# Optimization experiments

Measured on AMD Instinct MI355X. Metric: run time of the kernel, lower is better.

The kernel has to match this reference:

```python
import jax, jax.numpy as jnp
import numpy as np

N, C, H, W = 4, 256, 32, 32
NH = 2                      # att_nhead
HD = C // NH                # 128 per-head dim
MAX_DIS = 7
WS = 2 * MAX_DIS + 1        # 15 window side
WW = WS * WS                # 225 window positions
T = (C / NH) ** 0.5


def _gather_idx(h, w):
    # idx[wpos, m]: flat index into zero-padded (h+14, w+14) grid of the
    # neighbor at window offset wpos for query pixel m (== F.unfold semantics)
    pw = w + 2 * MAX_DIS
    dy, dx = np.meshgrid(np.arange(WS), np.arange(WS), indexing='ij')
    ys, xs = np.meshgrid(np.arange(h), np.arange(w), indexing='ij')
    idx = (dy.reshape(-1, 1) + ys.reshape(1, -1)) * pw + (dx.reshape(-1, 1) + xs.reshape(1, -1))
    return jnp.asarray(idx, dtype=jnp.int32)  # [WW, h*w]


def setup_inputs() -> dict:
    key = jax.random.key(0)
    ks = jax.random.split(key, 14)
    s = 0.02
    return {
        'q': jax.random.normal(ks[0], (N, C, H, W), jnp.float32),
        'k': jax.random.normal(ks[1], (N, C, H, W), jnp.float32),
        'v': jax.random.normal(ks[2], (N, C, H, W), jnp.float32),
        'Wq': jax.random.normal(ks[3], (C, C), jnp.float32) * s,
        'bq': jnp.zeros((C,), jnp.float32),
        'Wk': jax.random.normal(ks[4], (C, C), jnp.float32) * s,
        'bk': jnp.zeros((C,), jnp.float32),
        'Wv': jax.random.normal(ks[5], (C, C), jnp.float32) * s,
        'bv': jnp.zeros((C,), jnp.float32),
        'Wrel': jax.random.normal(ks[6], (NH, WW, HD), jnp.float32) * s,   # grouped 1x1 conv
        'brel': jnp.zeros((NH * WW,), jnp.float32),
        'V_bias': jax.random.normal(ks[7], (NH, HD, WW), jnp.float32) * s,
        'Wfc': jax.random.normal(ks[8], (C, C), jnp.float32) * s,
        'bfc': jnp.zeros((C,), jnp.float32),
    }


def _conv1x1(x, Wt, b):
    return jnp.einsum('nchw,dc->ndhw', x, Wt) + b[None, :, None, None]


def reference(q, k, v, Wq, bq, Wk, bk, Wv, bv, Wrel, brel, V_bias, Wfc, bfc):
    n, c, h, w = q.shape
    hw = h * w
    idx = _gather_idx(h, w)                                   # [WW, hw]
    pad = ((0, 0), (0, 0), (0, 0), (MAX_DIS, MAX_DIS), (MAX_DIS, MAX_DIS))

    q = _conv1x1(q, Wq, bq)
    k = _conv1x1(k, Wk, bk)
    v = _conv1x1(v, Wv, bv)

    # grouped 1x1 conv: relative position logits, [n, NH, WW, hw]
    rel = jnp.einsum('ngcxy,gwc->ngwxy', q.reshape(n, NH, HD, h, w), Wrel)
    rel = rel + brel.reshape(NH, WW)[None, :, :, None, None]
    rel = rel.reshape(n, NH, WW, hw)

    qs = (q / T).reshape(n, NH, HD, hw)

    # unfold K via zero-pad + gather: [n, NH, HD, WW, hw]
    k_pad = jnp.pad(k.reshape(n, NH, HD, h, w), pad).reshape(n, NH, HD, -1)
    k_un = k_pad[..., idx]
    qk = jnp.einsum('ngcm,ngcwm->ngwm', qs, k_un) + rel

    # boundary mask: neighbor inside the original image
    valid = jnp.pad(jnp.ones((h, w), jnp.float32), MAX_DIS).reshape(-1)[idx] > 0
    qk = jnp.where(valid[None, None], qk, jnp.float32(-1e8))
    attn = jax.nn.softmax(qk, axis=2)                         # over window positions

    agg_bias = jnp.einsum('ngwm,gcw->mngc', attn, V_bias).reshape(hw, n, c)

    # local2global scatter + dense einsum == gather of zero-padded V
    v_pad = jnp.pad(v.reshape(n, NH, HD, h, w), pad).reshape(n, NH, HD, -1)
    v_un = v_pad[..., idx]                                    # [n, NH, HD, WW, hw]
    agg_value = jnp.einsum('ngwm,ngcwm->mngc', attn, v_un).reshape(hw, n, c)

    out = (agg_value + agg_bias) @ Wfc.T + bfc                # [hw, n, c]
    return out
```

## Files before the change

### kernel.cpp

```cpp
#include <hip/hip_runtime.h>
#include <math.h>


typedef __attribute__((ext_vector_type(8))) short short8;
typedef __attribute__((ext_vector_type(4))) short short4v;
typedef __attribute__((ext_vector_type(4))) float floatx4;

__device__ __forceinline__ short f2bf(float f) {
    unsigned u = __float_as_uint(f);
    unsigned r = (u + 0x7fffu + ((u >> 16) & 1u)) >> 16;
    return (short)r;
}
__device__ __forceinline__ float bf2f(short s) {
    return __uint_as_float(((unsigned)(unsigned short)s) << 16);
}

__global__ __launch_bounds__(64)
void conv_w(const float* __restrict__ Wq, const float* __restrict__ Wk,
            const float* __restrict__ Wv, const float* __restrict__ Wfc,
            const float* __restrict__ Wrel, const float* __restrict__ Vb,
            short* __restrict__ Whi, short* __restrict__ Wlo,
            short* __restrict__ Wrh, short* __restrict__ Wrl,
            short* __restrict__ Vbh, short* __restrict__ Vbl)
{
    const int lane = threadIdx.x;
    const int n16 = lane & 15, quad = lane >> 4;
    const int z = blockIdx.z;

    if (z < 4) {
        const float* W = (z == 0 ? Wq : z == 1 ? Wk : z == 2 ? Wv : Wfc);
        const int dt = blockIdx.x, kc = blockIdx.y;
        const int d = dt * 16 + n16, cb = kc * 32 + quad * 8;
        float4 w0 = *(const float4*)&W[d * 256 + cb];
        float4 w1 = *(const float4*)&W[d * 256 + cb + 4];
        float f[8] = {w0.x, w0.y, w0.z, w0.w, w1.x, w1.y, w1.z, w1.w};
        short8 h8, l8;
#pragma unroll
        for (int j = 0; j < 8; ++j) {
            short hb = f2bf(f[j]);
            h8[j] = hb;
            l8[j] = f2bf(f[j] - bf2f(hb));
        }
        long off = (long)z * 65536 + (((long)(dt * 8 + kc) * 64) + lane) * 8;
        *(short8*)(Whi + off) = h8;
        *(short8*)(Wlo + off) = l8;
    } else if (z < 6) {
        const int g = z - 4;
        const int wt = blockIdx.x, kc = blockIdx.y;
        if (wt >= 15 || kc >= 4) return;
        const int w = wt * 16 + n16;
        const int cb = kc * 32 + quad * 8;
        float f[8] = {0.f, 0.f, 0.f, 0.f, 0.f, 0.f, 0.f, 0.f};
        if (w < 225) {
            float4 w0 = *(const float4*)&Wrel[(long)(g * 225 + w) * 128 + cb];
            float4 w1 = *(const float4*)&Wrel[(long)(g * 225 + w) * 128 + cb + 4];
            f[0] = w0.x; f[1] = w0.y; f[2] = w0.z; f[3] = w0.w;
            f[4] = w1.x; f[5] = w1.y; f[6] = w1.z; f[7] = w1.w;
        }
        short8 h8, l8;
#pragma unroll
        for (int j = 0; j < 8; ++j) {
            short hb = f2bf(f[j]);
            h8[j] = hb;
            l8[j] = f2bf(f[j] - bf2f(hb));
        }
        long off = (long)g * 30720 + (((long)(wt * 4 + kc) * 64) + lane) * 8;
        *(short8*)(Wrh + off) = h8;
        *(short8*)(Wrl + off) = l8;
    } else {
        const int g = z - 6;
        const int dt = blockIdx.x, wk = blockIdx.y;
        if (dt >= 8) return;
        const int ch = dt * 16 + n16;
        const int w0 = wk * 32 + quad * 8;
        float f[8];
#pragma unroll
        for (int j = 0; j < 8; ++j) {
            int w = w0 + j;
            f[j] = (w < 225) ? Vb[(long)(g * 128 + ch) * 225 + w] : 0.f;
        }
        short8 h8, l8;
#pragma unroll
        for (int j = 0; j < 8; ++j) {
            short hb = f2bf(f[j]);
            h8[j] = hb;
            l8[j] = f2bf(f[j] - bf2f(hb));
        }
        long off = (((long)(g * 128 + ch)) << 8) + w0;
        *(short8*)(Vbh + off) = h8;
        *(short8*)(Vbl + off) = l8;
    }
}

__global__ __launch_bounds__(256)
void mfma_proj(const float* __restrict__ q, const float* __restrict__ k,
               const float* __restrict__ v,
               const short* __restrict__ Whi, const short* __restrict__ Wlo,
               const float* __restrict__ bq, const float* __restrict__ bk,
               const float* __restrict__ bv,
               short* __restrict__ qhi, short* __restrict__ qlo,
               short* __restrict__ khi, short* __restrict__ klo,
               short* __restrict__ vhi, short* __restrict__ vlo)
{
    __shared__ float st[256 * 17];
    const int tid = threadIdx.x;
    const int wave = tid >> 6, lane = tid & 63;
    const int n16 = lane & 15, quad = lane >> 4;
    const int mt16 = blockIdx.x, z = blockIdx.y;
    const int sel = z >> 2, batch = z & 3;

    const float* X = (sel == 0 ? q : sel == 1 ? k : v) + ((long)batch << 18);

    {
        const float* src = X + ((long)tid << 10) + mt16 * 16;
        float4 a0 = *(const float4*)(src);
        float4 a1 = *(const float4*)(src + 4);
        float4 a2 = *(const float4*)(src + 8);
        float4 a3 = *(const float4*)(src + 12);
        float* d = &st[tid * 17];
        d[0] = a0.x; d[1] = a0.y; d[2] = a0.z; d[3] = a0.w;
        d[4] = a1.x; d[5] = a1.y; d[6] = a1.z; d[7] = a1.w;
        d[8] = a2.x; d[9] = a2.y; d[10] = a2.z; d[11] = a2.w;
        d[12] = a3.x; d[13] = a3.y; d[14] = a3.z; d[15] = a3.w;
    }

    const float* bias = (sel == 0 ? bq : sel == 1 ? bk : bv);
    float bbv[4][4];
#pragma unroll
    for (int i = 0; i < 4; ++i) {
        float4 b4 = *(const float4*)&bias[(wave * 4 + i) * 16 + quad * 4];
        bbv[i][0] = b4.x; bbv[i][1] = b4.y; bbv[i][2] = b4.z; bbv[i][3] = b4.w;
    }
    __syncthreads();

    floatx4 acc[4] = {{0.f,0.f,0.f,0.f},{0.f,0.f,0.f,0.f},
                      {0.f,0.f,0.f,0.f},{0.f,0.f,0.f,0.f}};
    const long abase = (long)sel * 65536 + (long)lane * 8;
#pragma unroll
    for (int kc = 0; kc < 8; ++kc) {
        short8 bh, bl;
        const float* col = &st[(kc * 32 + quad * 8) * 17 + n16];
#pragma unroll
        for (int j = 0; j < 8; ++j) {
            float f = col[j * 17];
            short hb = f2bf(f);
            bh[j] = hb;
            bl[j] = f2bf(f - bf2f(hb));
        }
#pragma unroll
        for (int i = 0; i < 4; ++i) {
            const int dt = wave * 4 + i;
            short8 ahi = *(const short8*)(Whi + abase + (long)(dt * 8 + kc) * 512);
            short8 alo = *(const short8*)(Wlo + abase + (long)(dt * 8 + kc) * 512);
            acc[i] = __builtin_amdgcn_mfma_f32_16x16x32_bf16(ahi, bh, acc[i], 0, 0, 0);
            acc[i] = __builtin_amdgcn_mfma_f32_16x16x32_bf16(ahi, bl, acc[i], 0, 0, 0);
            acc[i] = __builtin_amdgcn_mfma_f32_16x16x32_bf16(alo, bh, acc[i], 0, 0, 0);
        }
    }

    if (sel == 2) {
        const int m = mt16 * 16 + n16;
        const int yq = m >> 5, col = (m & 31) + 8;
#pragma unroll
        for (int i = 0; i < 4; ++i) {
            const int dt = wave * 4 + i;
#pragma unroll
            for (int r = 0; r < 4; ++r) {
                const int ch = dt * 16 + quad * 4 + r;
                const int gg = ch >> 7, chh = ch & 127;
                float f = acc[i][r] + bbv[i][r];
                short hb = f2bf(f);
                short lb = f2bf(f - bf2f(hb));
                long o = (((long)((batch * 2 + gg) * 128 + chh) * 32 + yq)) * 48 + col;
                vhi[o] = hb;
                vlo[o] = lb;
            }
        }
        {
            const int prow = mt16 >> 1, side = mt16 & 1;
            const int gg = tid >> 7, chp = tid & 127;
            long po = (((long)((batch * 2 + gg) * 128 + chp) * 32 + prow)) * 48 + side * 40;
            short8 zz = {0,0,0,0,0,0,0,0};
            *(short8*)(vhi + po) = zz;
            *(short8*)(vlo + po) = zz;
        }
        return;
    }

    __syncthreads();
    float* tile = st;
#pragma unroll
    for (int i = 0; i < 4; ++i) {
        const int dt = wave * 4 + i;
#pragma unroll
        for (int r = 0; r < 4; ++r)
            tile[n16 * 257 + dt * 16 + quad * 4 + r] = acc[i][r] + bbv[i][r];
    }
    __syncthreads();

    const float scale = (sel == 1) ? 0.08838834764831845f : 1.0f;
    const int m_l = tid >> 4, c16 = (tid & 15) * 16;
    const int m = mt16 * 16 + m_l;
    short* oh = sel ? khi : qhi;
    short* ol = sel ? klo : qlo;
#pragma unroll
    for (int half = 0; half < 2; ++half) {
        const int cg = c16 + half * 8;
        short8 h8, l8;
#pragma unroll
        for (int j = 0; j < 8; ++j) {
            float f = tile[m_l * 257 + cg + j] * scale;
            short hb = f2bf(f);
            h8[j] = hb;
            l8[j] = f2bf(f - bf2f(hb));
        }
        const int g = cg >> 7, ch = cg & 127;
        const long base = (((long)(batch * 2 + g) << 10) + m) * 128 + ch;
        *(short8*)(oh + base) = h8;
        *(short8*)(ol + base) = l8;
    }
}

__global__ __launch_bounds__(256)
void scores_pv(const short* __restrict__ qhi, const short* __restrict__ qlo,
               const short* __restrict__ khi, const short* __restrict__ klo,
               const short* __restrict__ Wrh, const short* __restrict__ Wrl,
               const float* __restrict__ brel,
               const short* __restrict__ vhi, const short* __restrict__ vlo,
               const short* __restrict__ Vbh, const short* __restrict__ Vbl,
               short* __restrict__ AGhi, short* __restrict__ AGlo)
{
    __shared__ __align__(16) float qk[16 * 241];
    __shared__ __align__(16) short pah[16 * 264];
    __shared__ __align__(16) short pal[16 * 264];
    __shared__ float invl[16];

    const int tid = threadIdx.x;
    const int wave = tid >> 6, lane = tid & 63;
    const int lin = blockIdx.x;
    const int bz  = lin & 7;
    const int yy  = lin >> 3;
    const int y   = yy >> 1;
    const int xt  = yy & 1;
    const int g = bz & 1;
    const int x0 = xt * 16;

    const int n16 = lane & 15, quad = lane >> 4;
    const long qbase = (((long)bz << 10) + y * 32 + x0 + n16) * 128 + quad * 8;
    short8 a_hi[4], a_lo[4];
#pragma unroll
    for (int ch = 0; ch < 4; ++ch) {
        a_hi[ch] = *(const short8*)(qhi + qbase + ch * 32);
        a_lo[ch] = *(const short8*)(qlo + qbase + ch * 32);
    }

    for (int wt = wave; wt < 15; wt += 4) {
        const short* Ah = Wrh + (long)g * 30720 + ((long)(wt * 4) * 64 + lane) * 8;
        const short* Al = Wrl + (long)g * 30720 + ((long)(wt * 4) * 64 + lane) * 8;
        floatx4 racc = {0.f, 0.f, 0.f, 0.f};
#pragma unroll
        for (int kc = 0; kc < 4; ++kc) {
            short8 whh = *(const short8*)(Ah + kc * 512);
            short8 wll = *(const short8*)(Al + kc * 512);
            racc = __builtin_amdgcn_mfma_f32_16x16x32_bf16(whh, a_hi[kc], racc, 0, 0, 0);
            racc = __builtin_amdgcn_mfma_f32_16x16x32_bf16(whh, a_lo[kc], racc, 0, 0, 0);
            racc = __builtin_amdgcn_mfma_f32_16x16x32_bf16(wll, a_hi[kc], racc, 0, 0, 0);
        }
#pragma unroll
        for (int r = 0; r < 4; ++r) {
            int w = wt * 16 + quad * 4 + r;
            if (w < 225) {
                int dy = w / 15, dx = w - dy * 15;
                qk[n16 * 241 + dy * 16 + dx] = racc[r] + brel[g * 225 + w];
            }
        }
    }
    __syncthreads();

    for (int e = tid; e < 16 * 241; e += 256) {
        int px = e / 241, idx = e - px * 241;
        int dy = idx >> 4, dx = idx & 15;
        int hy = y + dy - 7, hx = x0 + px + dx - 7;
        bool valid = (dx < 15) && (dy < 15) &&
                     (hy >= 0) && (hy < 32) && (hx >= 0) && (hx < 32);
        if (!valid) qk[e] = -1e8f;
    }
    __syncthreads();

    for (int dy = wave; dy < 15; dy += 4) {
        const int ky = y + dy - 7;
        if (ky < 0 || ky > 31) continue;
#pragma unroll
        for (int kxt = 0; kxt < 2; ++kxt) {
            const int kxg = x0 - 8 + kxt * 16 + n16;
            const long kb = (((long)bz << 10) + ky * 32 + kxg) * 128 + quad * 8;
            floatx4 acc = {0.f, 0.f, 0.f, 0.f};
#pragma unroll
            for (int ch = 0; ch < 4; ++ch) {
                short8 b_hi = *(const short8*)(khi + kb + ch * 32);
                short8 b_lo = *(const short8*)(klo + kb + ch * 32);
                acc = __builtin_amdgcn_mfma_f32_16x16x32_bf16(a_hi[ch], b_hi, acc, 0, 0, 0);
                acc = __builtin_amdgcn_mfma_f32_16x16x32_bf16(a_hi[ch], b_lo, acc, 0, 0, 0);
                acc = __builtin_amdgcn_mfma_f32_16x16x32_bf16(a_lo[ch], b_hi, acc, 0, 0, 0);
            }
            if (kxg >= 0 && kxg < 32) {
#pragma unroll
                for (int r = 0; r < 4; ++r) {
                    int m = quad * 4 + r;
                    int dx = kxg - (x0 + m) + 7;
                    if (dx >= 0 && dx < 15) {
                        int s = m * 241 + dy * 16 + dx;
                        qk[s] = qk[s] + acc[r];
                    }
                }
            }
        }
    }
    __syncthreads();

    {
        int px = tid >> 4, s = tid & 15;
        float mx = -3.0e38f;
        for (int w = s; w < 240; w += 16) mx = fmaxf(mx, qk[px * 241 + w]);
#pragma unroll
        for (int msk = 8; msk; msk >>= 1) mx = fmaxf(mx, __shfl_xor(mx, msk));
        float sum = 0.f;
        for (int w = s; w < 240; w += 16) {
            float p = __expf(qk[px * 241 + w] - mx);
            qk[px * 241 + w] = p;
            sum += p;
        }
#pragma unroll
        for (int msk = 8; msk; msk >>= 1) sum += __shfl_xor(sum, msk);
        if (s == 0) invl[px] = 1.0f / sum;
    }
    __syncthreads();

    for (int e = tid; e < 4096; e += 256) {
        int px = e >> 8, w = e & 255;
        float p = 0.f;
        if (w < 225) {
            int dy2 = w / 15, dx2 = w - dy2 * 15;
            p = qk[px * 241 + dy2 * 16 + dx2] * invl[px];
        }
        short hb = f2bf(p);
        pah[px * 264 + w] = hb;
        pal[px * 264 + w] = f2bf(p - bf2f(hb));
    }
    __syncthreads();

    floatx4 acc[2] = {{0.f,0.f,0.f,0.f},{0.f,0.f,0.f,0.f}};
    const int ch0a = (wave * 2) * 16;
    const int ch0b = (wave * 2 + 1) * 16;

#pragma unroll
    for (int wk = 0; wk < 8; ++wk) {
        short8 pa_h = *(const short8*)&pah[n16 * 264 + wk * 32 + quad * 8];
        short8 pa_l = *(const short8*)&pal[n16 * 264 + wk * 32 + quad * 8];
        const long vb0 = (((long)(g * 128 + ch0a + n16)) << 8) + wk * 32 + quad * 8;
        const long vb1 = (((long)(g * 128 + ch0b + n16)) << 8) + wk * 32 + quad * 8;
        short8 b0h = *(const short8*)(Vbh + vb0);
        short8 b0l = *(const short8*)(Vbl + vb0);
        short8 b1h = *(const short8*)(Vbh + vb1);
        short8 b1l = *(const short8*)(Vbl + vb1);
        acc[0] = __builtin_amdgcn_mfma_f32_16x16x32_bf16(pa_h, b0h, acc[0], 0, 0, 0);
        acc[0] = __builtin_amdgcn_mfma_f32_16x16x32_bf16(pa_h, b0l, acc[0], 0, 0, 0);
        acc[0] = __builtin_amdgcn_mfma_f32_16x16x32_bf16(pa_l, b0h, acc[0], 0, 0, 0);
        acc[1] = __builtin_amdgcn_mfma_f32_16x16x32_bf16(pa_h, b1h, acc[1], 0, 0, 0);
        acc[1] = __builtin_amdgcn_mfma_f32_16x16x32_bf16(pa_h, b1l, acc[1], 0, 0, 0);
        acc[1] = __builtin_amdgcn_mfma_f32_16x16x32_bf16(pa_l, b1h, acc[1], 0, 0, 0);
    }

    for (int dy = 0; dy < 15; ++dy) {
        const int ky = y + dy - 7;
        if (ky < 0 || ky > 31) continue;
        short8 bnd_h, bnd_l;
        const int rowoff = n16 * 264 + dy * 15 - n16 - 1;
#pragma unroll
        for (int j = 0; j < 8; ++j) {
            int kk = quad * 8 + j;
            int dx = kk - n16 - 1;
            bool valid = (unsigned)dx < 15u;
            int idx = valid ? (rowoff + kk) : 0;
            short vh = pah[idx];
            short vl = pal[idx];
            bnd_h[j] = valid ? vh : (short)0;
            bnd_l[j] = valid ? vl : (short)0;
        }
        const long v0o = (((long)((bz * 128 + ch0a + n16)) * 32 + ky)) * 48 + x0 + quad * 8;
        const long v1o = (((long)((bz * 128 + ch0b + n16)) * 32 + ky)) * 48 + x0 + quad * 8;
        short8 v0h = *(const short8*)(vhi + v0o);
        short8 v0l = *(const short8*)(vlo + v0o);
        short8 v1h = *(const short8*)(vhi + v1o);
        short8 v1l = *(const short8*)(vlo + v1o);
        acc[0] = __builtin_amdgcn_mfma_f32_16x16x32_bf16(bnd_h, v0h, acc[0], 0, 0, 0);
        acc[0] = __builtin_amdgcn_mfma_f32_16x16x32_bf16(bnd_h, v0l, acc[0], 0, 0, 0);
        acc[0] = __builtin_amdgcn_mfma_f32_16x16x32_bf16(bnd_l, v0h, acc[0], 0, 0, 0);
        acc[1] = __builtin_amdgcn_mfma_f32_16x16x32_bf16(bnd_h, v1h, acc[1], 0, 0, 0);
        acc[1] = __builtin_amdgcn_mfma_f32_16x16x32_bf16(bnd_h, v1l, acc[1], 0, 0, 0);
        acc[1] = __builtin_amdgcn_mfma_f32_16x16x32_bf16(bnd_l, v1h, acc[1], 0, 0, 0);
    }

    float* tile = qk;
#pragma unroll
    for (int t = 0; t < 2; ++t) {
        const int cb = (wave * 2 + t) * 16 + n16;
#pragma unroll
        for (int r = 0; r < 4; ++r)
            tile[(quad * 4 + r) * 133 + cb] = acc[t][r];
    }
    __syncthreads();

    const int sub = tid >> 6;
    short8 h8, l8;
#pragma unroll
    for (int j = 0; j < 8; ++j) {
        float f = tile[n16 * 133 + sub * 32 + quad * 8 + j];
        short hb = f2bf(f);
        h8[j] = hb;
        l8[j] = f2bf(f - bf2f(hb));
    }
    const int n = bz >> 1;
    const int mt16 = y * 2 + xt;
    const int kc = g * 4 + sub;
    long off = (long)n * 262144 + (((long)(mt16 * 8 + kc) * 64) + lane) * 8;
    *(short8*)(AGhi + off) = h8;
    *(short8*)(AGlo + off) = l8;
}

__global__ __launch_bounds__(256)
void mfma_fc(const short* __restrict__ Ahi, const short* __restrict__ Alo,
             const short* __restrict__ Whi, const short* __restrict__ Wlo,
             const float* __restrict__ bfc, float* __restrict__ out)
{
    __shared__ float tile[16 * 132];
    const int tid = threadIdx.x;
    const int wave = tid >> 6, lane = tid & 63;
    const int n16 = lane & 15, quad = lane >> 4;
    const int mt16 = blockIdx.x, db2 = blockIdx.y, nz = blockIdx.z;
    const int dt0 = db2 * 8 + wave * 2;

    const short* Bh = Ahi + (long)nz * 262144;
    const short* Bl = Alo + (long)nz * 262144;
    const long abase = (long)3 * 65536 + (long)lane * 8;

    float bbv[2][4];
#pragma unroll
    for (int p = 0; p < 2; ++p) {
        float4 b4 = *(const float4*)&bfc[(dt0 + p) * 16 + quad * 4];
        bbv[p][0] = b4.x; bbv[p][1] = b4.y; bbv[p][2] = b4.z; bbv[p][3] = b4.w;
    }

    floatx4 acc[2] = {{0.f,0.f,0.f,0.f},{0.f,0.f,0.f,0.f}};
#pragma unroll
    for (int kc = 0; kc < 8; ++kc) {
        const long bo = (long)(mt16 * 8 + kc) * 512 + (long)lane * 8;
        short8 bh = *(const short8*)(Bh + bo);
        short8 bl = *(const short8*)(Bl + bo);
#pragma unroll
        for (int p = 0; p < 2; ++p) {
            const int dt = dt0 + p;
            short8 ahi = *(const short8*)(Whi + abase + (long)(dt * 8 + kc) * 512);
            short8 alo = *(const short8*)(Wlo + abase + (long)(dt * 8 + kc) * 512);
            acc[p] = __builtin_amdgcn_mfma_f32_16x16x32_bf16(ahi, bh, acc[p], 0, 0, 0);
            acc[p] = __builtin_amdgcn_mfma_f32_16x16x32_bf16(ahi, bl, acc[p], 0, 0, 0);
            acc[p] = __builtin_amdgcn_mfma_f32_16x16x32_bf16(alo, bh, acc[p], 0, 0, 0);
        }
    }

#pragma unroll
    for (int p = 0; p < 2; ++p) {
        const int dl = (wave * 2 + p) * 16 + quad * 4;
#pragma unroll
        for (int r = 0; r < 4; ++r)
            tile[n16 * 132 + dl + r] = acc[p][r] + bbv[p][r];
    }
    __syncthreads();

    const int m_l = tid >> 4, d8 = (tid & 15) * 8;
    float4 o0 = *(const float4*)&tile[m_l * 132 + d8];
    float4 o1 = *(const float4*)&tile[m_l * 132 + d8 + 4];
    long ob = (long)(mt16 * 16 + m_l) * 1024 + nz * 256 + db2 * 128 + d8;
    *(float4*)&out[ob] = o0;
    *(float4*)&out[ob + 4] = o1;
}

extern "C" void kernel_launch(void* const* d_in, const int* in_sizes, int n_in,
                              void* d_out, int out_size, void* d_ws, size_t ws_size,
                              hipStream_t stream)
{
    const float* q    = (const float*)d_in[0];
    const float* k    = (const float*)d_in[1];
    const float* v    = (const float*)d_in[2];
    const float* Wq   = (const float*)d_in[3];
    const float* bq   = (const float*)d_in[4];
    const float* Wk   = (const float*)d_in[5];
    const float* bk   = (const float*)d_in[6];
    const float* Wv   = (const float*)d_in[7];
    const float* bv   = (const float*)d_in[8];
    const float* Wrel = (const float*)d_in[9];
    const float* brel = (const float*)d_in[10];
    const float* Vb   = (const float*)d_in[11];
    const float* Wfc  = (const float*)d_in[12];
    const float* bfc  = (const float*)d_in[13];
    float* out = (float*)d_out;

    float* ws   = (float*)d_ws;
    short* vhi  = (short*)(ws + 2097152);
    short* vlo  = (short*)(ws + 2883584);
    short* Vbh  = (short*)(ws + 4718592);
    short* Vbl  = (short*)(ws + 4751360);
    short* qhi  = (short*)(ws + 6561792);
    short* qlo  = (short*)(ws + 7086080);
    short* khi  = (short*)(ws + 7610368);
    short* klo  = (short*)(ws + 8134656);
    short* Whi  = (short*)(ws + 11804672);
    short* Wlo  = (short*)(ws + 11935744);
    short* AGhi = (short*)(ws + 12066816);
    short* AGlo = (short*)(ws + 12591104);
    short* Wrh  = (short*)(ws + 13115392);
    short* Wrl  = (short*)(ws + 13146112);

    conv_w<<<dim3(16, 8, 8), dim3(64), 0, stream>>>(Wq, Wk, Wv, Wfc, Wrel, Vb,
                                                    Whi, Wlo, Wrh, Wrl, Vbh, Vbl);

    mfma_proj<<<dim3(64, 12), dim3(256), 0, stream>>>(q, k, v, Whi, Wlo,
                                                      bq, bk, bv,
                                                      qhi, qlo, khi, klo,
                                                      vhi, vlo);

    scores_pv<<<dim3(512), dim3(256), 0, stream>>>(qhi, qlo, khi, klo,
                                                   Wrh, Wrl, brel,
                                                   vhi, vlo, Vbh, Vbl,
                                                   AGhi, AGlo);

    mfma_fc<<<dim3(64, 2, 4), dim3(256), 0, stream>>>(AGhi, AGlo, Whi, Wlo,
                                                      bfc, out);
}
```

Baseline: 162.4 us.

## Split attention channels across blocks, hoist QK MFMAs, vectorize V store

```diff
diff --git a/kernel.cpp b/kernel.cpp
--- a/kernel.cpp
+++ b/kernel.cpp
@@ -158,35 +158,6 @@
         }
     }
 
-    if (sel == 2) {
-        const int m = mt16 * 16 + n16;
-        const int yq = m >> 5, col = (m & 31) + 8;
-#pragma unroll
-        for (int i = 0; i < 4; ++i) {
-            const int dt = wave * 4 + i;
-#pragma unroll
-            for (int r = 0; r < 4; ++r) {
-                const int ch = dt * 16 + quad * 4 + r;
-                const int gg = ch >> 7, chh = ch & 127;
-                float f = acc[i][r] + bbv[i][r];
-                short hb = f2bf(f);
-                short lb = f2bf(f - bf2f(hb));
-                long o = (((long)((batch * 2 + gg) * 128 + chh) * 32 + yq)) * 48 + col;
-                vhi[o] = hb;
-                vlo[o] = lb;
-            }
-        }
-        {
-            const int prow = mt16 >> 1, side = mt16 & 1;
-            const int gg = tid >> 7, chp = tid & 127;
-            long po = (((long)((batch * 2 + gg) * 128 + chp) * 32 + prow)) * 48 + side * 40;
-            short8 zz = {0,0,0,0,0,0,0,0};
-            *(short8*)(vhi + po) = zz;
-            *(short8*)(vlo + po) = zz;
-        }
-        return;
-    }
-
     __syncthreads();
     float* tile = st;
 #pragma unroll
@@ -197,6 +168,31 @@
             tile[n16 * 257 + dt * 16 + quad * 4 + r] = acc[i][r] + bbv[i][r];
     }
     __syncthreads();
+
+    if (sel == 2) {
+        const int gg = tid >> 7, chp = tid & 127;
+        const int yq = mt16 >> 1, xb = (mt16 & 1) * 16;
+        short8 h0, h1, l0, l1;
+#pragma unroll
+        for (int j = 0; j < 8; ++j) {
+            float f0 = tile[j * 257 + tid];
+            float f1 = tile[(j + 8) * 257 + tid];
+            short hb0 = f2bf(f0), hb1 = f2bf(f1);
+            h0[j] = hb0; l0[j] = f2bf(f0 - bf2f(hb0));
+            h1[j] = hb1; l1[j] = f2bf(f1 - bf2f(hb1));
+        }
+        long o = ((long)((batch * 2 + gg) * 128 + chp) * 32 + yq) * 48 + 8 + xb;
+        *(short8*)(vhi + o) = h0;
+        *(short8*)(vhi + o + 8) = h1;
+        *(short8*)(vlo + o) = l0;
+        *(short8*)(vlo + o + 8) = l1;
+        const int prow = mt16 >> 1, side = mt16 & 1;
+        long po = ((long)((batch * 2 + gg) * 128 + chp) * 32 + prow) * 48 + side * 40;
+        short8 zz = {0,0,0,0,0,0,0,0};
+        *(short8*)(vhi + po) = zz;
+        *(short8*)(vlo + po) = zz;
+        return;
+    }
 
     const float scale = (sel == 1) ? 0.08838834764831845f : 1.0f;
     const int m_l = tid >> 4, c16 = (tid & 15) * 16;
@@ -239,7 +235,9 @@
     const int wave = tid >> 6, lane = tid & 63;
     const int lin = blockIdx.x;
     const int bz  = lin & 7;
-    const int yy  = lin >> 3;
+    const int r2  = lin >> 3;
+    const int chh = r2 & 1;
+    const int yy  = r2 >> 1;
     const int y   = yy >> 1;
     const int xt  = yy & 1;
     const int g = bz & 1;
@@ -252,6 +250,34 @@
     for (int ch = 0; ch < 4; ++ch) {
         a_hi[ch] = *(const short8*)(qhi + qbase + ch * 32);
         a_lo[ch] = *(const short8*)(qlo + qbase + ch * 32);
+    }
+
+    floatx4 bacc[4][2];
+#pragma unroll
+    for (int i = 0; i < 4; ++i)
+#pragma unroll
+        for (int t = 0; t < 2; ++t)
+            bacc[i][t] = (floatx4){0.f, 0.f, 0.f, 0.f};
+
+#pragma unroll
+    for (int i = 0; i < 4; ++i) {
+        const int dy = wave + i * 4;
+        const int ky = y + dy - 7;
+        if (dy < 15 && ky >= 0 && ky <= 31) {
+#pragma unroll
+            for (int kxt = 0; kxt < 2; ++kxt) {
+                const int kxg = x0 - 8 + kxt * 16 + n16;
+                const long kb = (((long)bz << 10) + ky * 32 + kxg) * 128 + quad * 8;
+#pragma unroll
+                for (int ch = 0; ch < 4; ++ch) {
+                    short8 b_hi = *(const short8*)(khi + kb + ch * 32);
+                    short8 b_lo = *(const short8*)(klo + kb + ch * 32);
+                    bacc[i][kxt] = __builtin_amdgcn_mfma_f32_16x16x32_bf16(a_hi[ch], b_hi, bacc[i][kxt], 0, 0, 0);
+                    bacc[i][kxt] = __builtin_amdgcn_mfma_f32_16x16x32_bf16(a_hi[ch], b_lo, bacc[i][kxt], 0, 0, 0);
+                    bacc[i][kxt] = __builtin_amdgcn_mfma_f32_16x16x32_bf16(a_lo[ch], b_hi, bacc[i][kxt], 0, 0, 0);
+                }
+            }
+        }
     }
 
     for (int wt = wave; wt < 15; wt += 4) {
@@ -277,40 +303,23 @@
     }
     __syncthreads();
 
-    for (int e = tid; e < 16 * 241; e += 256) {
-        int px = e / 241, idx = e - px * 241;
-        int dy = idx >> 4, dx = idx & 15;
-        int hy = y + dy - 7, hx = x0 + px + dx - 7;
-        bool valid = (dx < 15) && (dy < 15) &&
-                     (hy >= 0) && (hy < 32) && (hx >= 0) && (hx < 32);
-        if (!valid) qk[e] = -1e8f;
-    }
-    __syncthreads();
-
-    for (int dy = wave; dy < 15; dy += 4) {
+#pragma unroll
+    for (int i = 0; i < 4; ++i) {
+        const int dy = wave + i * 4;
         const int ky = y + dy - 7;
-        if (ky < 0 || ky > 31) continue;
-#pragma unroll
-        for (int kxt = 0; kxt < 2; ++kxt) {
-            const int kxg = x0 - 8 + kxt * 16 + n16;
-            const long kb = (((long)bz << 10) + ky * 32 + kxg) * 128 + quad * 8;
-            floatx4 acc = {0.f, 0.f, 0.f, 0.f};
-#pragma unroll
-            for (int ch = 0; ch < 4; ++ch) {
-                short8 b_hi = *(const short8*)(khi + kb + ch * 32);
-                short8 b_lo = *(const short8*)(klo + kb + ch * 32);
-                acc = __builtin_amdgcn_mfma_f32_16x16x32_bf16(a_hi[ch], b_hi, acc, 0, 0, 0);
-                acc = __builtin_amdgcn_mfma_f32_16x16x32_bf16(a_hi[ch], b_lo, acc, 0, 0, 0);
-                acc = __builtin_amdgcn_mfma_f32_16x16x32_bf16(a_lo[ch], b_hi, acc, 0, 0, 0);
-            }
-            if (kxg >= 0 && kxg < 32) {
-#pragma unroll
-                for (int r = 0; r < 4; ++r) {
-                    int m = quad * 4 + r;
-                    int dx = kxg - (x0 + m) + 7;
-                    if (dx >= 0 && dx < 15) {
-                        int s = m * 241 + dy * 16 + dx;
-                        qk[s] = qk[s] + acc[r];
+        if (dy < 15 && ky >= 0 && ky <= 31) {
+#pragma unroll
+            for (int kxt = 0; kxt < 2; ++kxt) {
+                const int kxg = x0 - 8 + kxt * 16 + n16;
+                if (kxg >= 0 && kxg < 32) {
+#pragma unroll
+                    for (int r = 0; r < 4; ++r) {
+                        int m = quad * 4 + r;
+                        int dx = kxg - (x0 + m) + 7;
+                        if (dx >= 0 && dx < 15) {
+                            int s = m * 241 + dy * 16 + dx;
+                            qk[s] = qk[s] + bacc[i][kxt][r];
+                        }
                     }
                 }
             }
@@ -321,13 +330,23 @@
     {
         int px = tid >> 4, s = tid & 15;
         float mx = -3.0e38f;
-        for (int w = s; w < 240; w += 16) mx = fmaxf(mx, qk[px * 241 + w]);
+        for (int w = s; w < 225; w += 16) {
+            int dy = w / 15, dx = w - dy * 15;
+            int hy = y + dy - 7, hx = x0 + px + dx - 7;
+            bool valid = (hy >= 0) && (hy < 32) && (hx >= 0) && (hx < 32);
+            float v = qk[px * 241 + dy * 16 + dx];
+            if (valid) mx = fmaxf(mx, v);
+        }
 #pragma unroll
         for (int msk = 8; msk; msk >>= 1) mx = fmaxf(mx, __shfl_xor(mx, msk));
         float sum = 0.f;
-        for (int w = s; w < 240; w += 16) {
-            float p = __expf(qk[px * 241 + w] - mx);
-            qk[px * 241 + w] = p;
+        for (int w = s; w < 225; w += 16) {
+            int dy = w / 15, dx = w - dy * 15;
+            int hy = y + dy - 7, hx = x0 + px + dx - 7;
+            bool valid = (hy >= 0) && (hy < 32) && (hx >= 0) && (hx < 32);
+            int slot = px * 241 + dy * 16 + dx;
+            float p = valid ? __expf(qk[slot] - mx) : 0.f;
+            qk[slot] = p;
             sum += p;
         }
 #pragma unroll
@@ -349,26 +368,19 @@
     }
     __syncthreads();
 
-    floatx4 acc[2] = {{0.f,0.f,0.f,0.f},{0.f,0.f,0.f,0.f}};
-    const int ch0a = (wave * 2) * 16;
-    const int ch0b = (wave * 2 + 1) * 16;
+    floatx4 acc = {0.f, 0.f, 0.f, 0.f};
+    const int ch0 = chh * 64 + wave * 16;
 
 #pragma unroll
     for (int wk = 0; wk < 8; ++wk) {
         short8 pa_h = *(const short8*)&pah[n16 * 264 + wk * 32 + quad * 8];
         short8 pa_l = *(const short8*)&pal[n16 * 264 + wk * 32 + quad * 8];
-        const long vb0 = (((long)(g * 128 + ch0a + n16)) << 8) + wk * 32 + quad * 8;
-        const long vb1 = (((long)(g * 128 + ch0b + n16)) << 8) + wk * 32 + quad * 8;
+        const long vb0 = (((long)(g * 128 + ch0 + n16)) << 8) + wk * 32 + quad * 8;
         short8 b0h = *(const short8*)(Vbh + vb0);
         short8 b0l = *(const short8*)(Vbl + vb0);
-        short8 b1h = *(const short8*)(Vbh + vb1);
-        short8 b1l = *(const short8*)(Vbl + vb1);
-        acc[0] = __builtin_amdgcn_mfma_f32_16x16x32_bf16(pa_h, b0h, acc[0], 0, 0, 0);
-        acc[0] = __builtin_amdgcn_mfma_f32_16x16x32_bf16(pa_h, b0l, acc[0], 0, 0, 0);
-        acc[0] = __builtin_amdgcn_mfma_f32_16x16x32_bf16(pa_l, b0h, acc[0], 0, 0, 0);
-        acc[1] = __builtin_amdgcn_mfma_f32_16x16x32_bf16(pa_h, b1h, acc[1], 0, 0, 0);
-        acc[1] = __builtin_amdgcn_mfma_f32_16x16x32_bf16(pa_h, b1l, acc[1], 0, 0, 0);
-        acc[1] = __builtin_amdgcn_mfma_f32_16x16x32_bf16(pa_l, b1h, acc[1], 0, 0, 0);
+        acc = __builtin_amdgcn_mfma_f32_16x16x32_bf16(pa_h, b0h, acc, 0, 0, 0);
+        acc = __builtin_amdgcn_mfma_f32_16x16x32_bf16(pa_h, b0l, acc, 0, 0, 0);
+        acc = __builtin_amdgcn_mfma_f32_16x16x32_bf16(pa_l, b0h, acc, 0, 0, 0);
     }
 
     for (int dy = 0; dy < 15; ++dy) {
@@ -387,45 +399,40 @@
             bnd_h[j] = valid ? vh : (short)0;
             bnd_l[j] = valid ? vl : (short)0;
         }
-        const long v0o = (((long)((bz * 128 + ch0a + n16)) * 32 + ky)) * 48 + x0 + quad * 8;
-        const long v1o = (((long)((bz * 128 + ch0b + n16)) * 32 + ky)) * 48 + x0 + quad * 8;
+        const long v0o = (((long)((bz * 128 + ch0 + n16)) * 32 + ky)) * 48 + x0 + quad * 8;
         short8 v0h = *(const short8*)(vhi + v0o);
         short8 v0l = *(const short8*)(vlo + v0o);
-        short8 v1h = *(const short8*)(vhi + v1o);
-        short8 v1l = *(const short8*)(vlo + v1o);
-        acc[0] = __builtin_amdgcn_mfma_f32_16x16x32_bf16(bnd_h, v0h, acc[0], 0, 0, 0);
-        acc[0] = __builtin_amdgcn_mfma_f32_16x16x32_bf16(bnd_h, v0l, acc[0], 0, 0, 0);
-        acc[0] = __builtin_amdgcn_mfma_f32_16x16x32_bf16(bnd_l, v0h, acc[0], 0, 0, 0);
-        acc[1] = __builtin_amdgcn_mfma_f32_16x16x32_bf16(bnd_h, v1h, acc[1], 0, 0, 0);
-        acc[1] = __builtin_amdgcn_mfma_f32_16x16x32_bf16(bnd_h, v1l, acc[1], 0, 0, 0);
-        acc[1] = __builtin_amdgcn_mfma_f32_16x16x32_bf16(bnd_l, v1h, acc[1], 0, 0, 0);
+        acc = __builtin_amdgcn_mfma_f32_16x16x32_bf16(bnd_h, v0h, acc, 0, 0, 0);
+        acc = __builtin_amdgcn_mfma_f32_16x16x32_bf16(bnd_h, v0l, acc, 0, 0, 0);
+        acc = __builtin_amdgcn_mfma_f32_16x16x32_bf16(bnd_l, v0h, acc, 0, 0, 0);
     }
 
     float* tile = qk;
-#pragma unroll
-    for (int t = 0; t < 2; ++t) {
-        const int cb = (wave * 2 + t) * 16 + n16;
+    {
+        const int cb = wave * 16 + n16;
 #pragma unroll
         for (int r = 0; r < 4; ++r)
-            tile[(quad * 4 + r) * 133 + cb] = acc[t][r];
+            tile[(quad * 4 + r) * 68 + cb] = acc[r];
     }
     __syncthreads();
 
     const int sub = tid >> 6;
-    short8 h8, l8;
-#pragma unroll
-    for (int j = 0; j < 8; ++j) {
-        float f = tile[n16 * 133 + sub * 32 + quad * 8 + j];
-        short hb = f2bf(f);
-        h8[j] = hb;
-        l8[j] = f2bf(f - bf2f(hb));
-    }
-    const int n = bz >> 1;
-    const int mt16 = y * 2 + xt;
-    const int kc = g * 4 + sub;
-    long off = (long)n * 262144 + (((long)(mt16 * 8 + kc) * 64) + lane) * 8;
-    *(short8*)(AGhi + off) = h8;
-    *(short8*)(AGlo + off) = l8;
+    if (sub < 2) {
+        short8 h8, l8;
+#pragma unroll
+        for (int j = 0; j < 8; ++j) {
+            float f = tile[n16 * 68 + sub * 32 + quad * 8 + j];
+            short hb = f2bf(f);
+            h8[j] = hb;
+            l8[j] = f2bf(f - bf2f(hb));
+        }
+        const int n = bz >> 1;
+        const int mt16 = y * 2 + xt;
+        const int kc = g * 4 + chh * 2 + sub;
+        long off = (long)n * 262144 + (((long)(mt16 * 8 + kc) * 64) + lane) * 8;
+        *(short8*)(AGhi + off) = h8;
+        *(short8*)(AGlo + off) = l8;
+    }
 }
 
 __global__ __launch_bounds__(256)
@@ -433,56 +440,43 @@
              const short* __restrict__ Whi, const short* __restrict__ Wlo,
              const float* __restrict__ bfc, float* __restrict__ out)
 {
-    __shared__ float tile[16 * 132];
+    __shared__ float tile[16 * 68];
     const int tid = threadIdx.x;
     const int wave = tid >> 6, lane = tid & 63;
     const int n16 = lane & 15, quad = lane >> 4;
-    const int mt16 = blockIdx.x, db2 = blockIdx.y, nz = blockIdx.z;
-    const int dt0 = db2 * 8 + wave * 2;
-
+    const int mt16 = blockIdx.x, db = blockIdx.y, nz = blockIdx.z;
+    const int dt = db * 4 + wave;
+
+    const short* Ah = Whi + (long)3 * 65536 + ((long)(dt * 8) * 64 + lane) * 8;
+    const short* Al = Wlo + (long)3 * 65536 + ((long)(dt * 8) * 64 + lane) * 8;
     const short* Bh = Ahi + (long)nz * 262144;
     const short* Bl = Alo + (long)nz * 262144;
-    const long abase = (long)3 * 65536 + (long)lane * 8;
-
-    float bbv[2][4];
-#pragma unroll
-    for (int p = 0; p < 2; ++p) {
-        float4 b4 = *(const float4*)&bfc[(dt0 + p) * 16 + quad * 4];
-        bbv[p][0] = b4.x; bbv[p][1] = b4.y; bbv[p][2] = b4.z; bbv[p][3] = b4.w;
-    }
-
-    floatx4 acc[2] = {{0.f,0.f,0.f,0.f},{0.f,0.f,0.f,0.f}};
+
+    float4 bv4 = *(const float4*)&bfc[dt * 16 + quad * 4];
+    float bb[4] = {bv4.x, bv4.y, bv4.z, bv4.w};
+
+    floatx4 acc = {0.f, 0.f, 0.f, 0.f};
 #pragma unroll
     for (int kc = 0; kc < 8; ++kc) {
-        const long bo = (long)(mt16 * 8 + kc) * 512 + (long)lane * 8;
+        short8 ahi = *(const short8*)(Ah + kc * 512);
+        short8 alo = *(const short8*)(Al + kc * 512);
+        long bo = ((long)(mt16 * 8 + kc) * 64 + lane) * 8;
         short8 bh = *(const short8*)(Bh + bo);
         short8 bl = *(const short8*)(Bl + bo);
-#pragma unroll
-        for (int p = 0; p < 2; ++p) {
-            const int dt = dt0 + p;
-            short8 ahi = *(const short8*)(Whi + abase + (long)(dt * 8 + kc) * 512);
-            short8 alo = *(const short8*)(Wlo + abase + (long)(dt * 8 + kc) * 512);
-            acc[p] = __builtin_amdgcn_mfma_f32_16x16x32_bf16(ahi, bh, acc[p], 0, 0, 0);
-            acc[p] = __builtin_amdgcn_mfma_f32_16x16x32_bf16(ahi, bl, acc[p], 0, 0, 0);
-            acc[p] = __builtin_amdgcn_mfma_f32_16x16x32_bf16(alo, bh, acc[p], 0, 0, 0);
-        }
-    }
-
-#pragma unroll
-    for (int p = 0; p < 2; ++p) {
-        const int dl = (wave * 2 + p) * 16 + quad * 4;
-#pragma unroll
-        for (int r = 0; r < 4; ++r)
-            tile[n16 * 132 + dl + r] = acc[p][r] + bbv[p][r];
-    }
-    __syncthreads();
-
-    const int m_l = tid >> 4, d8 = (tid & 15) * 8;
-    float4 o0 = *(const float4*)&tile[m_l * 132 + d8];
-    float4 o1 = *(const float4*)&tile[m_l * 132 + d8 + 4];
-    long ob = (long)(mt16 * 16 + m_l) * 1024 + nz * 256 + db2 * 128 + d8;
-    *(float4*)&out[ob] = o0;
-    *(float4*)&out[ob + 4] = o1;
+        acc = __builtin_amdgcn_mfma_f32_16x16x32_bf16(ahi, bh, acc, 0, 0, 0);
+        acc = __builtin_amdgcn_mfma_f32_16x16x32_bf16(ahi, bl, acc, 0, 0, 0);
+        acc = __builtin_amdgcn_mfma_f32_16x16x32_bf16(alo, bh, acc, 0, 0, 0);
+    }
+
+    const int dl = wave * 16 + quad * 4;
+#pragma unroll
+    for (int r = 0; r < 4; ++r)
+        tile[n16 * 68 + dl + r] = acc[r] + bb[r];
+    __syncthreads();
+
+    const int mm = tid >> 4, d4 = (tid & 15) * 4;
+    float4 o4 = *(const float4*)&tile[mm * 68 + d4];
+    *(float4*)&out[(long)(mt16 * 16 + mm) * 1024 + nz * 256 + db * 64 + d4] = o4;
 }
 
 extern "C" void kernel_launch(void* const* d_in, const int* in_sizes, int n_in,
@@ -529,11 +523,11 @@
                                                       qhi, qlo, khi, klo,
                                                       vhi, vlo);
 
-    scores_pv<<<dim3(512), dim3(256), 0, stream>>>(qhi, qlo, khi, klo,
-                                                   Wrh, Wrl, brel,
-                                                   vhi, vlo, Vbh, Vbl,
-                                                   AGhi, AGlo);
-
-    mfma_fc<<<dim3(64, 2, 4), dim3(256), 0, stream>>>(AGhi, AGlo, Whi, Wlo,
+    scores_pv<<<dim3(1024), dim3(256), 0, stream>>>(qhi, qlo, khi, klo,
+                                                    Wrh, Wrl, brel,
+                                                    vhi, vlo, Vbh, Vbl,
+                                                    AGhi, AGlo);
+
+    mfma_fc<<<dim3(64, 4, 4), dim3(256), 0, stream>>>(AGhi, AGlo, Whi, Wlo,
                                                       bfc, out);
 }
```

Result: slower. 185.2 us (+14.0%).
